# Optimization experiments

Measured on AMD Instinct MI355X. Metric: run time of the kernel, lower is better.

## Reference

```python
import jax, jax.numpy as jnp
import numpy as np

NBINS = 100


def setup_inputs() -> dict:
    key = jax.random.key(0)
    x = jax.random.uniform(key, (64, 1048576), dtype=jnp.float32)  # values in [0,1)
    locs = jnp.arange(0.0, 1.0, 1.0 / NBINS, dtype=jnp.float32)   # [NBINS] bin centers (buffer)
    return {"x": x, "locs": locs}


def reference(x, locs):
    # Triangular-kernel soft histogram. Scan over bins so we never materialize
    # an [N, NBINS] intermediate; each step is one fused pass over x.
    r = 1.0 / locs.shape[0]  # kernel half-width

    def body(carry, loc):
        ct = jnp.maximum(r - jnp.abs(x - loc), 0.0).sum()
        return carry, ct

    _, counts = jax.lax.scan(body, None, locs)  # [NBINS]
    # norm=True branch
    return counts / (counts.sum() + 1e-6)
```

## Files before the change

### kernel.cpp

```cpp
#include <hip/hip_runtime.h>

#define NBINS 100
#define NROWS 101
#define BLK   64
#define GRID  1536
#define REP   8

typedef unsigned int       u32;
typedef unsigned long long u64;


__global__ void histo_zero(u64* __restrict__ g) {
    int i = blockIdx.x * blockDim.x + threadIdx.x;
    if (i < REP * NBINS) g[i] = 0ull;
}

__global__ __launch_bounds__(BLK) void histo_accum(const float* __restrict__ x,
                                                   u64* __restrict__ g,
                                                   int n4, int n) {
    __shared__ u32 h[NROWS * BLK];
    const int lane = threadIdx.x;

    for (int i = lane; i < NROWS * BLK; i += BLK) h[i] = 0u;
    __syncthreads();

#define PROC2(va, vb) {                                        \
        u32 u0 = (u32)((va) * 102400.0f + 0.5f);               \
        u32 u1 = (u32)((vb) * 102400.0f + 0.5f);               \
        u32 k0 = u0 >> 10, k1 = u1 >> 10;                      \
        u32 w0 = (1u << 20) + (u0 & 1023u);                    \
        u32 w1 = (1u << 20) + (u1 & 1023u);                    \
        bool eq = (k0 == k1);                                  \
        u32 w1m = w1 + (eq ? w0 : 0u);                         \
        u32 w0m = eq ? 0u : w0;                                \
        int a0 = (int)(k0 * BLK) + lane;                       \
        int a1 = (int)(k1 * BLK) + lane;                       \
        u32 d0 = h[a0];                                        \
        u32 d1 = h[a1];                                        \
        h[a0] = d0 + w0m;                                      \
        h[a1] = d1 + w1m;                                      \
    }

#define PROC1(va) {                                            \
        u32 u0 = (u32)((va) * 102400.0f + 0.5f);               \
        u32 k0 = u0 >> 10;                                     \
        int a0 = (int)(k0 * BLK) + lane;                       \
        h[a0] += (1u << 20) + (u0 & 1023u);                    \
    }

#define PROC2x2(v) { PROC2((v).x, (v).y); PROC2((v).z, (v).w); }

    const float4* __restrict__ x4 = (const float4*)x;
    const int stride = gridDim.x * BLK;
    int i = blockIdx.x * BLK + lane;

    for (; i + 7 * stride < n4; i += 8 * stride) {
        float4 v0 = x4[i];
        float4 v1 = x4[i + 1 * stride];
        float4 v2 = x4[i + 2 * stride];
        float4 v3 = x4[i + 3 * stride];
        float4 v4 = x4[i + 4 * stride];
        float4 v5 = x4[i + 5 * stride];
        float4 v6 = x4[i + 6 * stride];
        float4 v7 = x4[i + 7 * stride];
        PROC2x2(v0); PROC2x2(v1); PROC2x2(v2); PROC2x2(v3);
        PROC2x2(v4); PROC2x2(v5); PROC2x2(v6); PROC2x2(v7);
    }
    for (; i < n4; i += stride) {
        float4 v = x4[i];
        PROC2x2(v);
    }
    if (blockIdx.x == 0) {
        for (int t = n4 * 4 + lane; t < n; t += BLK) PROC1(x[t]);
    }
#undef PROC2x2
#undef PROC1
#undef PROC2

    __syncthreads();

    u64* grep = &g[(blockIdx.x & (REP - 1)) * NBINS];
    for (int b = lane; b < NBINS; b += BLK) {
        u32 Ns = 0, Ts = 0;
#pragma unroll
        for (int c = 0; c < BLK; ++c) {
            int cc = (c + lane) & (BLK - 1);
            u32 u = h[b * BLK + cc];
            Ns += u >> 20;
            Ts += u & 0xFFFFFu;
        }
        atomicAdd(&grep[b], ((u64)Ns << 37) + (u64)Ts);
    }
}

__global__ void histo_final(const u64* __restrict__ g, float* __restrict__ out) {
    __shared__ float Tprev[NBINS + 1];
    __shared__ float wsum[2];
    const int t = threadIdx.x;

    float N = 0.0f, T = 0.0f;
    if (t < NBINS) {
        u64 acc = 0ull;
#pragma unroll
        for (int r = 0; r < REP; ++r) acc += g[r * NBINS + t];
        N = (float)(acc >> 37);
        T = (float)(acc & ((1ull << 37) - 1ull));
        Tprev[t + 1] = T;
    }
    if (t == 127) Tprev[0] = 0.0f;
    __syncthreads();

    float c = 0.0f;
    if (t < NBINS) c = 0.01f * (N + (Tprev[t] - T) * (1.0f / 1024.0f));

    float s = c;
#pragma unroll
    for (int o = 32; o > 0; o >>= 1) s += __shfl_down(s, o, 64);
    if ((t & 63) == 0) wsum[t >> 6] = s;
    __syncthreads();

    float total = wsum[0] + wsum[1];
    if (t < NBINS) out[t] = c / (total + 1e-6f);
}

extern "C" void kernel_launch(void* const* d_in, const int* in_sizes, int n_in,
                              void* d_out, int out_size, void* d_ws, size_t ws_size,
                              hipStream_t stream) {
    const float* x   = (const float*)d_in[0];
    float*       out = (float*)d_out;
    u64*         g   = (u64*)d_ws;

    const int n  = in_sizes[0];
    const int n4 = n / 4;

    histo_zero<<<(REP * NBINS + 255) / 256, 256, 0, stream>>>(g);

    int blocks = GRID;
    int need   = (n4 + BLK - 1) / BLK;
    if (blocks > need) blocks = need;
    histo_accum<<<blocks, BLK, 0, stream>>>(x, g, n4, n);

    histo_final<<<1, 128, 0, stream>>>(g, out);
}
```

Before: 56.55 us.

## Double-buffer nontemporal loads and fuse finalization into last accumulating block

The main loop now software-pipelines two register batches of eight float4 loads, issuing the next batch before processing the current one, and uses nontemporal loads. The separate finalize kernel is removed: each block bumps a completion counter and the last block reads the replicated bins atomically and writes the normalized output. This aims to hide load latency and save one kernel launch, at the cost of higher register pressure and a threadfence/atomic per block.

```diff
diff --git a/kernel.cpp b/kernel.cpp
--- a/kernel.cpp
+++ b/kernel.cpp
@@ -8,17 +8,21 @@
 
 typedef unsigned int       u32;
 typedef unsigned long long u64;
+typedef float f32x4 __attribute__((ext_vector_type(4)));
 
 
 __global__ void histo_zero(u64* __restrict__ g) {
     int i = blockIdx.x * blockDim.x + threadIdx.x;
-    if (i < REP * NBINS) g[i] = 0ull;
+    if (i < REP * NBINS + 1) g[i] = 0ull;
 }
 
 __global__ __launch_bounds__(BLK) void histo_accum(const float* __restrict__ x,
                                                    u64* __restrict__ g,
-                                                   int n4, int n) {
-    __shared__ u32 h[NROWS * BLK];
+                                                   float* __restrict__ out,
+                                                   int n4, int n, int nblocks) {
+    __shared__ u32   h[NROWS * BLK];
+    __shared__ float Tsh[NBINS + 1];
+    __shared__ int   lastFlag;
     const int lane = threadIdx.x;
 
     for (int i = lane; i < NROWS * BLK; i += BLK) h[i] = 0u;
@@ -50,29 +54,55 @@
 
 #define PROC2x2(v) { PROC2((v).x, (v).y); PROC2((v).z, (v).w); }
 
-    const float4* __restrict__ x4 = (const float4*)x;
+#define LD8(Bk, p) {                                           \
+        Bk##0 = __builtin_nontemporal_load((p));               \
+        Bk##1 = __builtin_nontemporal_load((p) + 1 * stride);  \
+        Bk##2 = __builtin_nontemporal_load((p) + 2 * stride);  \
+        Bk##3 = __builtin_nontemporal_load((p) + 3 * stride);  \
+        Bk##4 = __builtin_nontemporal_load((p) + 4 * stride);  \
+        Bk##5 = __builtin_nontemporal_load((p) + 5 * stride);  \
+        Bk##6 = __builtin_nontemporal_load((p) + 6 * stride);  \
+        Bk##7 = __builtin_nontemporal_load((p) + 7 * stride);  \
+    }
+
+#define PR8(Bk) { PROC2x2(Bk##0); PROC2x2(Bk##1); PROC2x2(Bk##2); PROC2x2(Bk##3); \
+                  PROC2x2(Bk##4); PROC2x2(Bk##5); PROC2x2(Bk##6); PROC2x2(Bk##7); }
+
+    const f32x4* __restrict__ x4 = (const f32x4*)x;
     const int stride = gridDim.x * BLK;
-    int i = blockIdx.x * BLK + lane;
+    const int base   = blockIdx.x * BLK + lane;
 
-    for (; i + 7 * stride < n4; i += 8 * stride) {
-        float4 v0 = x4[i];
-        float4 v1 = x4[i + 1 * stride];
-        float4 v2 = x4[i + 2 * stride];
-        float4 v3 = x4[i + 3 * stride];
-        float4 v4 = x4[i + 4 * stride];
-        float4 v5 = x4[i + 5 * stride];
-        float4 v6 = x4[i + 6 * stride];
-        float4 v7 = x4[i + 7 * stride];
-        PROC2x2(v0); PROC2x2(v1); PROC2x2(v2); PROC2x2(v3);
-        PROC2x2(v4); PROC2x2(v5); PROC2x2(v6); PROC2x2(v7);
+    const int nfull = n4 / (8 * stride);
+    const f32x4* p  = x4 + base;
+
+    if (nfull >= 1) {
+        f32x4 A0, A1, A2, A3, A4, A5, A6, A7;
+        f32x4 B0, B1, B2, B3, B4, B5, B6, B7;
+        LD8(A, p); p += 8 * stride;
+        int grp = 1;
+        for (; grp + 1 < nfull; grp += 2) {
+            LD8(B, p); p += 8 * stride;
+            PR8(A);
+            LD8(A, p); p += 8 * stride;
+            PR8(B);
+        }
+        if (grp < nfull) {
+            LD8(B, p); p += 8 * stride;
+            PR8(A);
+            PR8(B);
+        } else {
+            PR8(A);
+        }
     }
-    for (; i < n4; i += stride) {
-        float4 v = x4[i];
+    for (int j = nfull * 8; base + j * stride < n4; ++j) {
+        f32x4 v = __builtin_nontemporal_load(x4 + base + j * stride);
         PROC2x2(v);
     }
     if (blockIdx.x == 0) {
-        for (int t = n4 * 4 + lane; t < n; t += BLK) PROC1(x[t]);
+        for (int t = n4 * 4 + lane; t < n; t += BLK) { float v = x[t]; PROC1(v); }
     }
+#undef PR8
+#undef LD8
 #undef PROC2x2
 #undef PROC1
 #undef PROC2
@@ -91,36 +121,41 @@
         }
         atomicAdd(&grep[b], ((u64)Ns << 37) + (u64)Ts);
     }
-}
 
-__global__ void histo_final(const u64* __restrict__ g, float* __restrict__ out) {
-    __shared__ float Tprev[NBINS + 1];
-    __shared__ float wsum[2];
-    const int t = threadIdx.x;
+    __threadfence();
+    if (lane == 0) {
+        u64 done = atomicAdd(&g[REP * NBINS], 1ull);
+        lastFlag = (done == (u64)(nblocks - 1));
+    }
+    __syncthreads();
+    if (!lastFlag) return;
+    __threadfence();
 
-    float N = 0.0f, T = 0.0f;
-    if (t < NBINS) {
-        u64 acc = 0ull;
+    u64 a0 = 0ull, a1 = 0ull;
 #pragma unroll
-        for (int r = 0; r < REP; ++r) acc += g[r * NBINS + t];
-        N = (float)(acc >> 37);
-        T = (float)(acc & ((1ull << 37) - 1ull));
-        Tprev[t + 1] = T;
+    for (int r = 0; r < REP; ++r) {
+        a0 += atomicAdd(&g[r * NBINS + lane], 0ull);
+        if (lane + 64 < NBINS) a1 += atomicAdd(&g[r * NBINS + lane + 64], 0ull);
     }
-    if (t == 127) Tprev[0] = 0.0f;
+    float N0 = (float)(a0 >> 37), T0 = (float)(a0 & ((1ull << 37) - 1ull));
+    float N1 = (float)(a1 >> 37), T1 = (float)(a1 & ((1ull << 37) - 1ull));
+
+    Tsh[lane + 1] = T0;
+    if (lane + 64 < NBINS) Tsh[lane + 65] = T1;
+    if (lane == 0) Tsh[0] = 0.0f;
     __syncthreads();
 
-    float c = 0.0f;
-    if (t < NBINS) c = 0.01f * (N + (Tprev[t] - T) * (1.0f / 1024.0f));
+    float c0 = 0.01f * (N0 + (Tsh[lane] - T0) * (1.0f / 1024.0f));
+    float c1 = (lane + 64 < NBINS)
+             ? 0.01f * (N1 + (Tsh[lane + 64] - T1) * (1.0f / 1024.0f)) : 0.0f;
 
-    float s = c;
+    float s = c0 + c1;
 #pragma unroll
     for (int o = 32; o > 0; o >>= 1) s += __shfl_down(s, o, 64);
-    if ((t & 63) == 0) wsum[t >> 6] = s;
-    __syncthreads();
+    s = __shfl(s, 0, 64);
 
-    float total = wsum[0] + wsum[1];
-    if (t < NBINS) out[t] = c / (total + 1e-6f);
+    out[lane] = c0 / (s + 1e-6f);
+    if (lane + 64 < NBINS) out[lane + 64] = c1 / (s + 1e-6f);
 }
 
 extern "C" void kernel_launch(void* const* d_in, const int* in_sizes, int n_in,
@@ -133,12 +168,10 @@
     const int n  = in_sizes[0];
     const int n4 = n / 4;
 
-    histo_zero<<<(REP * NBINS + 255) / 256, 256, 0, stream>>>(g);
+    histo_zero<<<(REP * NBINS + 1 + 255) / 256, 256, 0, stream>>>(g);
 
     int blocks = GRID;
     int need   = (n4 + BLK - 1) / BLK;
     if (blocks > need) blocks = need;
-    histo_accum<<<blocks, BLK, 0, stream>>>(x, g, n4, n);
-
-    histo_final<<<1, 128, 0, stream>>>(g, out);
+    histo_accum<<<blocks, BLK, 0, stream>>>(x, g, out, n4, n, blocks);
 }
```

Measured after the change: 108.3 us. 1.92x slower.
